# Kernel optimization log

Measured on AMD Instinct MI355X. Metric: run time of the kernel, lower is better.

Reference implementation:

```python
import jax, jax.numpy as jnp
import numpy as np

B, N, C = 4, 2048, 1024
H = 16
D = C // H  # head_dim = 64
SCALE = 1.0 / np.sqrt(D).astype(np.float32)


def setup_inputs() -> dict:
    key = jax.random.key(0)
    ks = jax.random.split(key, 6)
    s = 0.02
    return {
        "x": jax.random.normal(ks[0], (B, N, C), dtype=jnp.float32),
        "Wq": jax.random.normal(ks[1], (C, C), dtype=jnp.float32) * s,
        "Wk": jax.random.normal(ks[2], (C, C), dtype=jnp.float32) * s,
        "Wv": jax.random.normal(ks[3], (C, C), dtype=jnp.float32) * s,
        "Wo": jax.random.normal(ks[4], (C, C), dtype=jnp.float32) * s,
        "bo": jax.random.normal(ks[5], (C,), dtype=jnp.float32) * s,
    }


def reference(x, Wq, Wk, Wv, Wo, bo):
    # q/k/v projections (no bias, qkv_bias=False), split heads -> [B,H,N,D]
    def heads(t):
        return t.reshape(B, N, H, D).transpose(0, 2, 1, 3)
    q = heads(x @ Wq)
    k = heads(x @ Wk)
    v = heads(x @ Wv)
    attn = jnp.einsum("bhnd,bhmd->bhnm", q, k) * SCALE  # [B,H,N,N]
    attn = jax.nn.softmax(attn, axis=-1)
    out = jnp.einsum("bhnm,bhmd->bhnd", attn, v)  # [B,H,N,D]
    out = out.transpose(0, 2, 1, 3).reshape(B, N, C)
    return out @ Wo + bo
```

## Files before the change

### kernel.cpp

```cpp
#include <hip/hip_runtime.h>
#include <hip/hip_bf16.h>


typedef __bf16 bf16x8 __attribute__((ext_vector_type(8)));
typedef float  f32x4  __attribute__((ext_vector_type(4)));
typedef unsigned int u32x4 __attribute__((ext_vector_type(4)));

__device__ __forceinline__ f32x4 mfma16(bf16x8 a, bf16x8 b, f32x4 c) {
    return __builtin_amdgcn_mfma_f32_16x16x32_bf16(a, b, c, 0, 0, 0);
}

__device__ __forceinline__ unsigned short f2bf(float f) {
    unsigned u = __builtin_bit_cast(unsigned, f);
    u += 0x7fffu + ((u >> 16) & 1u);
    return (unsigned short)(u >> 16);
}

__device__ __forceinline__ unsigned cvt_pk_bf16(float lo, float hi) {
    unsigned r;
    asm("v_cvt_pk_bf16_f32 %0, %1, %2" : "=v"(r) : "v"(lo), "v"(hi));
    return r;
}

__device__ __forceinline__ void gload16(const ushort* g, ushort* l) {
    __builtin_amdgcn_global_load_lds(
        (const __attribute__((address_space(1))) void*)g,
        (__attribute__((address_space(3))) void*)l, 16, 0, 0);
}

__global__ void cast_bf16_kernel(const float4* __restrict__ in,
                                 ushort4* __restrict__ out, int n4) {
    int i = blockIdx.x * blockDim.x + threadIdx.x;
    if (i < n4) {
        float4 f = in[i];
        ushort4 r;
        r.x = f2bf(f.x); r.y = f2bf(f.y); r.z = f2bf(f.z); r.w = f2bf(f.w);
        out[i] = r;
    }
}

__global__ void transpose_cast_kernel(const float* __restrict__ Wq,
                                      const float* __restrict__ Wk,
                                      const float* __restrict__ Wv,
                                      const float* __restrict__ Wo,
                                      ushort* __restrict__ out) {
    __shared__ float tile[32][33];
    const int z = blockIdx.z;
    const float* W = (z == 0) ? Wq : (z == 1) ? Wk : (z == 2) ? Wv : Wo;
    ushort* o = out + (size_t)z * 1024 * 1024;
    const int k0 = blockIdx.x * 32, n0 = blockIdx.y * 32;
    const int tx = threadIdx.x, ty = threadIdx.y;
#pragma unroll
    for (int i = 0; i < 4; i++)
        tile[ty + 8 * i][tx] = W[(size_t)(k0 + ty + 8 * i) * 1024 + n0 + tx];
    __syncthreads();
#pragma unroll
    for (int i = 0; i < 4; i++)
        o[(size_t)(n0 + ty + 8 * i) * 1024 + k0 + tx] = f2bf(tile[tx][ty + 8 * i]);
}

template <int MODE>
__global__ __launch_bounds__(256) void gemm128(const ushort* __restrict__ A,
                                               const ushort* __restrict__ Bt,
                                               ushort* __restrict__ outB,
                                               float* __restrict__ outF,
                                               const float* __restrict__ bias) {
    __shared__ ushort As[128 * 32];
    __shared__ ushort Bs[128 * 32];
    const int tid = threadIdx.x;
    const int lane = tid & 63;
    const int wid = tid >> 6;
    const int wm = wid >> 1, wn = wid & 1;
    const int m0 = blockIdx.x * 128;
    const int n0 = blockIdx.y * 128;
    if (MODE == 0) Bt += (size_t)blockIdx.z * (1024 * 1024);

    f32x4 acc[4][4] = {};

    for (int k0 = 0; k0 < 1024; k0 += 32) {
#pragma unroll
        for (int it = 0; it < 2; ++it) {
            int e = (it * 256 + tid) * 8;
            int r = e >> 5, c = e & 31;
            gload16(&A[(size_t)(m0 + r) * 1024 + k0 + c], &As[e]);
            gload16(&Bt[(size_t)(n0 + r) * 1024 + k0 + c], &Bs[e]);
        }
        __syncthreads();

        bf16x8 a[4], b[4];
#pragma unroll
        for (int i = 0; i < 4; i++) {
            a[i] = *(const bf16x8*)&As[(wm * 64 + i * 16 + (lane & 15)) * 32 + (lane >> 4) * 8];
            b[i] = *(const bf16x8*)&Bs[(wn * 64 + i * 16 + (lane & 15)) * 32 + (lane >> 4) * 8];
        }
#pragma unroll
        for (int i = 0; i < 4; i++)
#pragma unroll
            for (int j = 0; j < 4; j++)
                acc[i][j] = mfma16(a[i], b[j], acc[i][j]);
        __syncthreads();
    }

#pragma unroll
    for (int i = 0; i < 4; i++) {
        int row_b = m0 + wm * 64 + i * 16 + ((lane >> 4) * 4);
#pragma unroll
        for (int j = 0; j < 4; j++) {
            int col = n0 + wn * 64 + j * 16 + (lane & 15);
#pragma unroll
            for (int r = 0; r < 4; r++) {
                int row = row_b + r;
                float v = acc[i][j][r];
                if (MODE == 0) {
                    ushort* o = outB + (size_t)blockIdx.z * (8192ull * 1024);
                    int b = row >> 11, n = row & 2047, h = col >> 6, d = col & 63;
                    o[((((size_t)(b * 16 + h)) * 2048 + n) << 6) + d] = f2bf(v);
                } else {
                    outF[(size_t)row * 1024 + col] = v + bias[col];
                }
            }
        }
    }
}

#define LSCALE 0.18033688f

__global__ __launch_bounds__(256) void attn_kernel(const ushort* __restrict__ Q,
                                                   const ushort* __restrict__ K,
                                                   const ushort* __restrict__ V,
                                                   ushort* __restrict__ O) {
    __shared__ ushort Ks[64 * 64];
    __shared__ ushort Vs[64 * 64];
    __shared__ ushort Ps[4][2][1024];
    const int tid = threadIdx.x;
    const int lane = tid & 63;
    const int wid = tid >> 6;
    const int g = lane >> 4;
    const int q16 = lane & 15;
    const int bid = blockIdx.x;
    const int swz = (bid & 7) * 128 + (bid >> 3);
    const int bh = swz >> 4;
    const int qt = swz & 15;
    const size_t base = (size_t)bh * (2048 * 64);

    const int qr0 = qt * 128 + wid * 32 + q16;
    bf16x8 qf[2][2];
#pragma unroll
    for (int u = 0; u < 2; ++u)
#pragma unroll
        for (int ks = 0; ks < 2; ++ks)
            qf[u][ks] = *(const bf16x8*)&Q[base + (size_t)(qr0 + u * 16) * 64 + ks * 32 + g * 8];

    bf16x8 onesb;
#pragma unroll
    for (int i = 0; i < 8; i++) onesb[i] = (__bf16)1.0f;

    f32x4 o[2][4] = {};
    f32x4 lacc[2] = {};
    float m_run[2] = {-1e30f, -1e30f};

    char* KsB = (char*)Ks;
    char* VsB = (char*)Vs;

    for (int kt = 0; kt < 2048; kt += 64) {
#pragma unroll
        for (int it = 0; it < 2; ++it) {
            int ci = it * 256 + tid;
            int key = ci >> 3, d0 = (ci & 7) * 8;
            uint4 kv = *(const uint4*)&K[base + (size_t)(kt + key) * 64 + d0];
            int byt = (key * 128 + d0 * 2) ^ ((key & 7) << 4);
            *(uint4*)(KsB + byt) = kv;

            int key2 = ci & 63;
            int d0v = (ci >> 6) * 8;
            uint4 vv = *(const uint4*)&V[base + (size_t)(kt + key2) * 64 + d0v];
            const ushort* vs = (const ushort*)&vv;
#pragma unroll
            for (int j = 0; j < 8; j++) {
                int d = d0v + j;
                int b2 = (d * 128 + key2 * 2) ^ ((d & 7) << 4);
                *(ushort*)(VsB + b2) = vs[j];
            }
        }
        __syncthreads();

        f32x4 s[2][4] = {};
#pragma unroll
        for (int kb = 0; kb < 4; ++kb) {
#pragma unroll
            for (int ks = 0; ks < 2; ++ks) {
                int key = kb * 16 + q16;
                int d0 = ks * 32 + g * 8;
                int byt = (key * 128 + d0 * 2) ^ ((key & 7) << 4);
                bf16x8 kf = *(const bf16x8*)(KsB + byt);
                s[0][kb] = mfma16(kf, qf[0][ks], s[0][kb]);
                s[1][kb] = mfma16(kf, qf[1][ks], s[1][kb]);
            }
        }

        bf16x8 pa[2][2];
#pragma unroll
        for (int u = 0; u < 2; ++u) {
            float t[4][4];
#pragma unroll
            for (int kb = 0; kb < 4; ++kb)
#pragma unroll
                for (int r = 0; r < 4; ++r) t[kb][r] = s[u][kb][r] * LSCALE;

            float mx = fmaxf(fmaxf(fmaxf(t[0][0], t[0][1]), fmaxf(t[0][2], t[0][3])),
                             fmaxf(fmaxf(t[1][0], t[1][1]), fmaxf(t[1][2], t[1][3])));
            mx = fmaxf(mx, fmaxf(fmaxf(fmaxf(t[2][0], t[2][1]), fmaxf(t[2][2], t[2][3])),
                                 fmaxf(fmaxf(t[3][0], t[3][1]), fmaxf(t[3][2], t[3][3]))));
            mx = fmaxf(mx, __shfl_xor(mx, 16));
            mx = fmaxf(mx, __shfl_xor(mx, 32));
            float mn = fmaxf(m_run[u], mx);
            float fr = __builtin_amdgcn_exp2f(m_run[u] - mn);
            m_run[u] = mn;

            unsigned w[4][2];
#pragma unroll
            for (int kb = 0; kb < 4; ++kb) {
                float p0 = __builtin_amdgcn_exp2f(t[kb][0] - mn);
                float p1 = __builtin_amdgcn_exp2f(t[kb][1] - mn);
                float p2 = __builtin_amdgcn_exp2f(t[kb][2] - mn);
                float p3 = __builtin_amdgcn_exp2f(t[kb][3] - mn);
                w[kb][0] = cvt_pk_bf16(p0, p1);
                w[kb][1] = cvt_pk_bf16(p2, p3);
            }

            char* PsB = (char*)Ps[wid][u];
            {
                u32x4 c0 = {w[0][0], w[0][1], w[2][0], w[2][1]};
                u32x4 c1 = {w[1][0], w[1][1], w[3][0], w[3][1]};
                *(u32x4*)(PsB + ((lane * 32 + 0)  ^ ((lane & 7) << 4))) = c0;
                *(u32x4*)(PsB + ((lane * 32 + 16) ^ ((lane & 7) << 4))) = c1;
            }
            asm volatile("" ::: "memory");
            __builtin_amdgcn_sched_barrier(0);
            int s1 = q16 + 32 * (g & 1);
            int ch = (g >> 1) * 16;
            u32x4 r1 = *(const u32x4*)(PsB + ((s1 * 32 + ch) ^ ((s1 & 7) << 4)));
            u32x4 r2 = *(const u32x4*)(PsB + (((s1 + 16) * 32 + ch) ^ (((s1 + 16) & 7) << 4)));
            asm volatile("" ::: "memory");
            {
                u32x4 p0 = {r1.x, r1.y, r2.x, r2.y};
                u32x4 p1 = {r1.z, r1.w, r2.z, r2.w};
                pa[u][0] = __builtin_bit_cast(bf16x8, p0);
                pa[u][1] = __builtin_bit_cast(bf16x8, p1);
            }

            float fro[4];
#pragma unroll
            for (int r = 0; r < 4; ++r) fro[r] = __shfl(fr, g * 4 + r);
#pragma unroll
            for (int cb = 0; cb < 4; ++cb)
#pragma unroll
                for (int r = 0; r < 4; ++r) o[u][cb][r] *= fro[r];
#pragma unroll
            for (int r = 0; r < 4; ++r) lacc[u][r] *= fro[r];

            lacc[u] = mfma16(pa[u][0], onesb, lacc[u]);
            lacc[u] = mfma16(pa[u][1], onesb, lacc[u]);
        }

#pragma unroll
        for (int cb = 0; cb < 4; ++cb) {
#pragma unroll
            for (int ks = 0; ks < 2; ++ks) {
                int d = cb * 16 + q16;
                int byt = (d * 128 + (ks * 32 + g * 8) * 2) ^ ((d & 7) << 4);
                bf16x8 vf = *(const bf16x8*)(VsB + byt);
                o[0][cb] = mfma16(pa[0][ks], vf, o[0][cb]);
                o[1][cb] = mfma16(pa[1][ks], vf, o[1][cb]);
            }
        }
        __syncthreads();
    }

    const int b = bh >> 4, h = bh & 15;
#pragma unroll
    for (int u = 0; u < 2; ++u) {
#pragma unroll
        for (int r = 0; r < 4; ++r) {
            float inv = 1.0f / lacc[u][r];
            int row = qt * 128 + wid * 32 + u * 16 + g * 4 + r;
#pragma unroll
            for (int cb = 0; cb < 4; ++cb) {
                int col = h * 64 + cb * 16 + q16;
                O[((size_t)(b * 2048 + row)) * 1024 + col] = f2bf(o[u][cb][r] * inv);
            }
        }
    }
}

extern "C" void kernel_launch(void* const* d_in, const int* in_sizes, int n_in,
                              void* d_out, int out_size, void* d_ws, size_t ws_size,
                              hipStream_t stream) {
    const float* x  = (const float*)d_in[0];
    const float* Wq = (const float*)d_in[1];
    const float* Wk = (const float*)d_in[2];
    const float* Wv = (const float*)d_in[3];
    const float* Wo = (const float*)d_in[4];
    const float* bo = (const float*)d_in[5];
    float* out = (float*)d_out;

    if (ws_size < (size_t)72 * 1024 * 1024) return;
    ushort* ws  = (ushort*)d_ws;
    ushort* xb  = ws;
    ushort* wt  = xb + (size_t)8 * 1024 * 1024;
    ushort* qkv = wt + (size_t)4 * 1024 * 1024;
    ushort* ao  = xb;

    cast_bf16_kernel<<<8192, 256, 0, stream>>>((const float4*)x, (ushort4*)xb,
                                               2 * 1024 * 1024);
    transpose_cast_kernel<<<dim3(32, 32, 4), dim3(32, 8), 0, stream>>>(Wq, Wk, Wv, Wo, wt);
    gemm128<0><<<dim3(64, 8, 3), 256, 0, stream>>>(xb, wt, qkv, nullptr, nullptr);
    attn_kernel<<<1024, 256, 0, stream>>>(
        qkv, qkv + (size_t)8 * 1024 * 1024, qkv + (size_t)16 * 1024 * 1024, ao);
    gemm128<1><<<dim3(64, 8, 1), 256, 0, stream>>>(ao, wt + (size_t)3 * 1024 * 1024,
                                                   nullptr, out, bo);
}
```

Measured before the change: 250.0 us.

## Load V via async global-to-LDS and use transposing LDS reads; fold softmax scale into Q

V tiles are no longer transposed with scalar 2-byte LDS stores. They are copied with global_load_lds in a 16-column-block layout and read back with ds_read_b64_tr_b16, which transposes during the LDS read to build MFMA B operands. The softmax log2 scale is now applied in the Q projection epilogue, which removes a per-score multiply in the attention loop. The change adds an explicit lgkmcnt wait and a sched barrier, and it depends on the transpose-read lane mapping matching the MFMA layout.

After: 242.0 us. -3.2%, faster.

```diff
diff --git a/kernel.cpp b/kernel.cpp
--- a/kernel.cpp
+++ b/kernel.cpp
@@ -3,8 +3,11 @@
 
 
 typedef __bf16 bf16x8 __attribute__((ext_vector_type(8)));
+typedef __bf16 bf16x4 __attribute__((ext_vector_type(4)));
 typedef float  f32x4  __attribute__((ext_vector_type(4)));
 typedef unsigned int u32x4 __attribute__((ext_vector_type(4)));
+
+#define LSCALE 0.18033688f
 
 __device__ __forceinline__ f32x4 mfma16(bf16x8 a, bf16x8 b, f32x4 c) {
     return __builtin_amdgcn_mfma_f32_16x16x32_bf16(a, b, c, 0, 0, 0);
@@ -20,6 +23,12 @@
     unsigned r;
     asm("v_cvt_pk_bf16_f32 %0, %1, %2" : "=v"(r) : "v"(lo), "v"(hi));
     return r;
+}
+
+__device__ __forceinline__ bf16x4 trread(unsigned addr) {
+    bf16x4 d;
+    asm volatile("ds_read_b64_tr_b16 %0, %1" : "=v"(d) : "v"(addr));
+    return d;
 }
 
 __device__ __forceinline__ void gload16(const ushort* g, ushort* l) {
@@ -101,6 +110,7 @@
         __syncthreads();
     }
 
+    const float scl = (MODE == 0 && blockIdx.z == 0) ? LSCALE : 1.0f;
 #pragma unroll
     for (int i = 0; i < 4; i++) {
         int row_b = m0 + wm * 64 + i * 16 + ((lane >> 4) * 4);
@@ -110,7 +120,7 @@
 #pragma unroll
             for (int r = 0; r < 4; r++) {
                 int row = row_b + r;
-                float v = acc[i][j][r];
+                float v = acc[i][j][r] * scl;
                 if (MODE == 0) {
                     ushort* o = outB + (size_t)blockIdx.z * (8192ull * 1024);
                     int b = row >> 11, n = row & 2047, h = col >> 6, d = col & 63;
@@ -122,8 +132,6 @@
         }
     }
 }
-
-#define LSCALE 0.18033688f
 
 __global__ __launch_bounds__(256) void attn_kernel(const ushort* __restrict__ Q,
                                                    const ushort* __restrict__ K,
@@ -160,7 +168,7 @@
     float m_run[2] = {-1e30f, -1e30f};
 
     char* KsB = (char*)Ks;
-    char* VsB = (char*)Vs;
+    const unsigned vb = (unsigned)(size_t)&Vs[0];
 
     for (int kt = 0; kt < 2048; kt += 64) {
 #pragma unroll
@@ -170,17 +178,13 @@
             uint4 kv = *(const uint4*)&K[base + (size_t)(kt + key) * 64 + d0];
             int byt = (key * 128 + d0 * 2) ^ ((key & 7) << 4);
             *(uint4*)(KsB + byt) = kv;
-
-            int key2 = ci & 63;
-            int d0v = (ci >> 6) * 8;
-            uint4 vv = *(const uint4*)&V[base + (size_t)(kt + key2) * 64 + d0v];
-            const ushort* vs = (const ushort*)&vv;
-#pragma unroll
-            for (int j = 0; j < 8; j++) {
-                int d = d0v + j;
-                int b2 = (d * 128 + key2 * 2) ^ ((d & 7) << 4);
-                *(ushort*)(VsB + b2) = vs[j];
-            }
+        }
+#pragma unroll
+        for (int it = 0; it < 2; ++it) {
+            int c = it * 256 + tid;
+            int key = (c & 127) >> 1;
+            int d0 = (c >> 7) * 16 + (c & 1) * 8;
+            gload16(&V[base + (size_t)(kt + key) * 64 + d0], &Vs[c * 8]);
         }
         __syncthreads();
 
@@ -205,7 +209,7 @@
 #pragma unroll
             for (int kb = 0; kb < 4; ++kb)
 #pragma unroll
-                for (int r = 0; r < 4; ++r) t[kb][r] = s[u][kb][r] * LSCALE;
+                for (int r = 0; r < 4; ++r) t[kb][r] = s[u][kb][r];
 
             float mx = fmaxf(fmaxf(fmaxf(t[0][0], t[0][1]), fmaxf(t[0][2], t[0][3])),
                              fmaxf(fmaxf(t[1][0], t[1][1]), fmaxf(t[1][2], t[1][3])));
@@ -263,17 +267,26 @@
             lacc[u] = mfma16(pa[u][1], onesb, lacc[u]);
         }
 
-#pragma unroll
-        for (int cb = 0; cb < 4; ++cb) {
+        bf16x4 vlo[4][2], vhi[4][2];
+#pragma unroll
+        for (int cb = 0; cb < 4; ++cb)
 #pragma unroll
             for (int ks = 0; ks < 2; ++ks) {
-                int d = cb * 16 + q16;
-                int byt = (d * 128 + (ks * 32 + g * 8) * 2) ^ ((d & 7) << 4);
-                bf16x8 vf = *(const bf16x8*)(VsB + byt);
+                unsigned a = vb + cb * 2048 + (ks * 32 + g * 8) * 32 + q16 * 8;
+                vlo[cb][ks] = trread(a);
+                vhi[cb][ks] = trread(a + 128);
+            }
+        asm volatile("s_waitcnt lgkmcnt(0)" ::: "memory");
+        __builtin_amdgcn_sched_barrier(0);
+#pragma unroll
+        for (int cb = 0; cb < 4; ++cb)
+#pragma unroll
+            for (int ks = 0; ks < 2; ++ks) {
+                bf16x8 vf = __builtin_shufflevector(vlo[cb][ks], vhi[cb][ks],
+                                                    0, 1, 2, 3, 4, 5, 6, 7);
                 o[0][cb] = mfma16(pa[0][ks], vf, o[0][cb]);
                 o[1][cb] = mfma16(pa[1][ks], vf, o[1][cb]);
             }
-        }
         __syncthreads();
     }
 
```
